# Optimization experiments

Measured on AMD Instinct MI355X. Metric: run time of the kernel, lower is better.

Reference implementation:

```python
import jax, jax.numpy as jnp
import numpy as np
from jax import lax


def _pairwise_dist(a, b):
    # a: (T, D), b: (T, D) -> (T, T) Euclidean distances via GEMM trick
    a2 = jnp.sum(a * a, axis=-1)
    b2 = jnp.sum(b * b, axis=-1)
    sq = a2[:, None] + b2[None, :] - 2.0 * (a @ b.T)
    return jnp.sqrt(jnp.maximum(sq, 1e-12))


def _frechet(seq1, seq2):
    cost = _pairwise_dist(seq1, seq2)  # (T, T)
    ca0 = lax.cummax(cost[0])          # first row boundary: running max

    def row_step(prev, cost_row):
        # prev: ca[i-1, :]; cost_row: cost[i, :]
        c0 = jnp.maximum(prev[0], cost_row[0])  # first-column boundary

        def col_step(left, x):
            c, up, diag = x
            val = jnp.maximum(c, jnp.minimum(jnp.minimum(up, left), diag))
            return val, val

        _, rest = lax.scan(col_step, c0, (cost_row[1:], prev[1:], prev[:-1]))
        cur = jnp.concatenate([c0[None], rest])
        return cur, None

    final_row, _ = lax.scan(row_step, ca0, cost[1:])
    return final_row[-1]


def setup_inputs() -> dict:
    key = jax.random.key(0)
    k1, k2 = jax.random.split(key)
    B, T, D = 32, 1024, 64
    pred = jax.random.normal(k1, (B, T, D), dtype=jnp.float32)
    targ = jax.random.normal(k2, (B, T, D), dtype=jnp.float32)
    return {"pred": pred, "targ": targ}


def reference(pred, targ):
    dists = jax.vmap(_frechet)(pred, targ)  # (B,)
    return jnp.mean(dists)
```

## Files before the change

kernel.cpp:

```cpp
#include <hip/hip_runtime.h>
#include <hip/hip_bf16.h>

#define T_LEN 1024
#define D_DIM 64
#define BATCH 32

#define BM 64
#define BN 128

__global__ __launch_bounds__(256, 3) void cost_kernel(const float* __restrict__ pred,
                                                      const float* __restrict__ targ,
                                                      float* __restrict__ cost) {
    const int b = blockIdx.z;
    const float* P = pred + (size_t)b * T_LEN * D_DIM;
    const float* Tg = targ + (size_t)b * T_LEN * D_DIM;
    float* C = cost + (size_t)b * T_LEN * T_LEN;
    const int row0 = blockIdx.y * BM;
    const int col0 = blockIdx.x * BN;

    __shared__ __align__(16) float ps[BM][D_DIM + 4];
    __shared__ __align__(16) float ts[D_DIM][BN + 4];
    __shared__ float p2[BM], t2[BN];

    const int tid = threadIdx.x;

#pragma unroll
    for (int it = 0; it < 4; ++it) {
        int f = tid + 256 * it;
        int row = f >> 4;
        int kc = f & 15;
        float4 v = *(const float4*)(P + (size_t)(row0 + row) * D_DIM + 4 * kc);
        *(float4*)&ps[row][4 * kc] = v;
    }
#pragma unroll
    for (int it = 0; it < 8; ++it) {
        int f = tid + 256 * it;
        int col = f >> 4;
        int kc = f & 15;
        float4 w = *(const float4*)(Tg + (size_t)(col0 + col) * D_DIM + 4 * kc);
        ts[4 * kc + 0][col] = w.x;
        ts[4 * kc + 1][col] = w.y;
        ts[4 * kc + 2][col] = w.z;
        ts[4 * kc + 3][col] = w.w;
    }
    __syncthreads();

    if (tid < 64) {
        float s = 0.0f;
        const float4* pr = (const float4*)&ps[tid][0];
#pragma unroll
        for (int q = 0; q < 16; ++q) {
            float4 v = pr[q];
            s += v.x * v.x; s += v.y * v.y; s += v.z * v.z; s += v.w * v.w;
        }
        p2[tid] = s;
    } else if (tid < 192) {
        int c = tid - 64;
        float s = 0.0f;
#pragma unroll
        for (int k = 0; k < 64; ++k) { float x = ts[k][c]; s += x * x; }
        t2[c] = s;
    }
    __syncthreads();

    const int tx = tid & 31;
    const int ty = tid >> 5;
    const int r0 = 8 * ty, c0 = 4 * tx;

    float acc[8][4];
#pragma unroll
    for (int i = 0; i < 8; ++i)
#pragma unroll
        for (int j = 0; j < 4; ++j) acc[i][j] = 0.0f;

#pragma unroll
    for (int k4 = 0; k4 < 16; ++k4) {
        float4 b0 = *(const float4*)&ts[4 * k4 + 0][c0];
        float4 b1 = *(const float4*)&ts[4 * k4 + 1][c0];
        float4 b2 = *(const float4*)&ts[4 * k4 + 2][c0];
        float4 b3 = *(const float4*)&ts[4 * k4 + 3][c0];
#pragma unroll
        for (int i = 0; i < 8; ++i) {
            float4 a = *(const float4*)&ps[r0 + i][4 * k4];
            acc[i][0] += a.x * b0.x; acc[i][1] += a.x * b0.y; acc[i][2] += a.x * b0.z; acc[i][3] += a.x * b0.w;
            acc[i][0] += a.y * b1.x; acc[i][1] += a.y * b1.y; acc[i][2] += a.y * b1.z; acc[i][3] += a.y * b1.w;
            acc[i][0] += a.z * b2.x; acc[i][1] += a.z * b2.y; acc[i][2] += a.z * b2.z; acc[i][3] += a.z * b2.w;
            acc[i][0] += a.w * b3.x; acc[i][1] += a.w * b3.y; acc[i][2] += a.w * b3.z; acc[i][3] += a.w * b3.w;
        }
    }

    float4 tt = *(const float4*)&t2[c0];
#pragma unroll
    for (int i = 0; i < 8; ++i) {
        float pa = p2[r0 + i];
        float4 o;
        o.x = sqrtf(fmaxf(pa + tt.x - 2.0f * acc[i][0], 1e-12f));
        o.y = sqrtf(fmaxf(pa + tt.y - 2.0f * acc[i][1], 1e-12f));
        o.z = sqrtf(fmaxf(pa + tt.z - 2.0f * acc[i][2], 1e-12f));
        o.w = sqrtf(fmaxf(pa + tt.w - 2.0f * acc[i][3], 1e-12f));
        *(float4*)(C + (size_t)(row0 + r0 + i) * T_LEN + (col0 + c0)) = o;
    }
}

#define PD 8

#define DP_LOAD4(D0, D1, D2, D3, SRC)                                         \
    asm volatile("global_load_dwordx4 %0, %4, off\n\t"                        \
                 "global_load_dwordx4 %1, %4, off offset:16\n\t"              \
                 "global_load_dwordx4 %2, %4, off offset:32\n\t"              \
                 "global_load_dwordx4 %3, %4, off offset:48"                  \
                 : "=&v"(D0), "=&v"(D1), "=&v"(D2), "=&v"(D3)                 \
                 : "v"(SRC))

__global__ __launch_bounds__(64) void dp_kernel(const float* __restrict__ cost,
                                                float* __restrict__ out) {
    const int b = blockIdx.x;
    const int t = threadIdx.x;
    const float INF = __builtin_inff();
    const float* C = cost + (size_t)b * T_LEN * T_LEN + 16 * t;

    float prev[16];
#pragma unroll
    for (int j = 0; j < 16; ++j) prev[j] = INF;
    float right_out = INF;
    float diag_feed = INF;

    float4 pipe[PD][4];

#pragma unroll
    for (int d = 0; d < PD; ++d) {
        int r = d - t; r = r < 0 ? 0 : (r > T_LEN - 1 ? T_LEN - 1 : r);
        const float* src = C + (size_t)r * T_LEN;
        DP_LOAD4(pipe[d][0], pipe[d][1], pipe[d][2], pipe[d][3], src);
    }

    const int S = T_LEN + 63;
    const int NCH = (S + PD - 1) / PD;
    int s = 0;

#define DP_STEP(U)                                                            \
    {                                                                         \
           \
        asm volatile("s_waitcnt vmcnt(28)" ::: "memory");                     \
        __builtin_amdgcn_sched_barrier(0);                                    \
        const float4 q0 = pipe[U][0], q1 = pipe[U][1];                        \
        const float4 q2 = pipe[U][2], q3 = pipe[U][3];                        \
        const int r = s - t;                                                  \
        float inc = __shfl_up(right_out, 1, 64);                              \
        float left = inc, diag = diag_feed;                                   \
        diag_feed = inc;                                                      \
        if (t == 0) { left = (r == 0) ? -INF : INF; diag = INF; }             \
        if (r >= 0 && r < T_LEN) {                                            \
            float cq[16] = {q0.x, q0.y, q0.z, q0.w, q1.x, q1.y, q1.z, q1.w,   \
                            q2.x, q2.y, q2.z, q2.w, q3.x, q3.y, q3.z, q3.w};  \
            float g[16];                                                      \
            g[0] = fmaxf(cq[0], fminf(prev[0], diag));                        \
            _Pragma("unroll")                                                 \
            for (int j = 1; j < 16; ++j)                                      \
                g[j] = fmaxf(cq[j], fminf(prev[j], prev[j - 1]));             \
            float v = left;                                                   \
            _Pragma("unroll")                                                 \
            for (int j = 0; j < 16; ++j) {                                    \
                v = __builtin_amdgcn_fmed3f(v, cq[j], g[j]);                  \
                prev[j] = v;                                                  \
            }                                                                 \
            right_out = v;                                                    \
        }                                                                     \
        __builtin_amdgcn_sched_barrier(0);                                    \
        {                                                                     \
            int rn = s + PD - t;                                              \
            rn = rn < 0 ? 0 : (rn > T_LEN - 1 ? T_LEN - 1 : rn);              \
            const float* src = C + (size_t)rn * T_LEN;                        \
            DP_LOAD4(pipe[U][0], pipe[U][1], pipe[U][2], pipe[U][3], src);    \
        }                                                                     \
        ++s;                                                                  \
    }

    for (int chunk = 0; chunk < NCH; ++chunk) {
        DP_STEP(0)
        DP_STEP(1)
        DP_STEP(2)
        DP_STEP(3)
        DP_STEP(4)
        DP_STEP(5)
        DP_STEP(6)
        DP_STEP(7)
    }
#undef DP_STEP

    asm volatile("s_waitcnt vmcnt(0)" ::: "memory");
    if (t == 63) atomicAdd(out, prev[15] * (1.0f / (float)BATCH));
}

__global__ __launch_bounds__(64) void dp_fused_kernel(const float* __restrict__ pred,
                                                      const float* __restrict__ targ,
                                                      float* __restrict__ out) {
    const int b = blockIdx.x;
    const int t = threadIdx.x;
    const float INF = __builtin_inff();
    const float* P = pred + (size_t)b * T_LEN * D_DIM;
    const float* T = targ + (size_t)b * T_LEN * D_DIM + (size_t)(16 * t) * D_DIM;

    float prev[16];
#pragma unroll
    for (int j = 0; j < 16; ++j) prev[j] = INF;
    float right_out = INF;
    float diag_feed = INF;

    for (int s = 0; s < T_LEN + 63; s++) {
        int r = s - t;
        float inc = __shfl_up(right_out, 1, 64);
        float left = inc, diag = diag_feed;
        diag_feed = inc;
        if (t == 0) { left = (r == 0) ? -INF : INF; diag = INF; }
        if (r >= 0 && r < T_LEN) {
            float4 pr[16];
            const float4* pp = (const float4*)(P + (size_t)r * D_DIM);
#pragma unroll
            for (int q = 0; q < 16; q++) pr[q] = pp[q];
#pragma unroll
            for (int j = 0; j < 16; j++) {
                const float4* tp = (const float4*)(T + (size_t)j * D_DIM);
                float acc = 0.0f;
#pragma unroll
                for (int q = 0; q < 16; q++) {
                    float4 tv = tp[q];
                    float dx = pr[q].x - tv.x; acc += dx * dx;
                    float dy = pr[q].y - tv.y; acc += dy * dy;
                    float dz = pr[q].z - tv.z; acc += dz * dz;
                    float dw = pr[q].w - tv.w; acc += dw * dw;
                }
                float c = sqrtf(fmaxf(acc, 1e-12f));
                float up = prev[j];
                float v = fmaxf(c, fminf(fminf(up, diag), left));
                diag = up; left = v; prev[j] = v;
            }
            right_out = left;
        }
    }
    if (t == 63) atomicAdd(out, prev[15] * (1.0f / (float)BATCH));
}

extern "C" void kernel_launch(void* const* d_in, const int* in_sizes, int n_in,
                              void* d_out, int out_size, void* d_ws, size_t ws_size,
                              hipStream_t stream) {
    const float* pred = (const float*)d_in[0];
    const float* targ = (const float*)d_in[1];
    float* out = (float*)d_out;

    hipMemsetAsync(out, 0, sizeof(float) * out_size, stream);

    const size_t per_batch = (size_t)T_LEN * T_LEN * sizeof(float);
    int bpg = (int)(ws_size / per_batch);
    if (bpg > BATCH) bpg = BATCH;

    if (bpg >= 1) {
        float* cost = (float*)d_ws;
        for (int g0 = 0; g0 < BATCH; g0 += bpg) {
            int gb = (BATCH - g0) < bpg ? (BATCH - g0) : bpg;
            dim3 grid(T_LEN / BN, T_LEN / BM, gb);
            cost_kernel<<<grid, 256, 0, stream>>>(pred + (size_t)g0 * T_LEN * D_DIM,
                                                  targ + (size_t)g0 * T_LEN * D_DIM,
                                                  cost);
            dp_kernel<<<gb, 64, 0, stream>>>(cost, out);
        }
    } else {
        dp_fused_kernel<<<BATCH, 64, 0, stream>>>(pred, targ, out);
    }
}
```

Before: 360.1 us.

## Enlarge cost GEMM tile to 128x128 and restructure DP pipeline registers

The cost kernel's row tile grows from 64 to 128, so each thread now computes an 8x8 register block instead of 8x4, and occupancy is lowered to 2 blocks. This raises arithmetic intensity and halves the number of target-tile reloads. The DP kernel swaps the pipe array for named float4 registers, moves the shuffle ahead of the waitcnt so its latency overlaps the pending loads, and sets launch bounds (64,1). The larger tile raises register and LDS pressure, which may reduce occupancy in the cost kernel.

```diff
diff --git a/kernel.cpp b/kernel.cpp
--- a/kernel.cpp
+++ b/kernel.cpp
@@ -5,10 +5,10 @@
 #define D_DIM 64
 #define BATCH 32
 
-#define BM 64
+#define BM 128
 #define BN 128
 
-__global__ __launch_bounds__(256, 3) void cost_kernel(const float* __restrict__ pred,
+__global__ __launch_bounds__(256, 2) void cost_kernel(const float* __restrict__ pred,
                                                       const float* __restrict__ targ,
                                                       float* __restrict__ cost) {
     const int b = blockIdx.z;
@@ -25,7 +25,7 @@
     const int tid = threadIdx.x;
 
 #pragma unroll
-    for (int it = 0; it < 4; ++it) {
+    for (int it = 0; it < 8; ++it) {
         int f = tid + 256 * it;
         int row = f >> 4;
         int kc = f & 15;
@@ -45,7 +45,7 @@
     }
     __syncthreads();
 
-    if (tid < 64) {
+    if (tid < 128) {
         float s = 0.0f;
         const float4* pr = (const float4*)&ps[tid][0];
 #pragma unroll
@@ -54,8 +54,8 @@
             s += v.x * v.x; s += v.y * v.y; s += v.z * v.z; s += v.w * v.w;
         }
         p2[tid] = s;
-    } else if (tid < 192) {
-        int c = tid - 64;
+    } else {
+        int c = tid - 128;
         float s = 0.0f;
 #pragma unroll
         for (int k = 0; k < 64; ++k) { float x = ts[k][c]; s += x * x; }
@@ -63,42 +63,72 @@
     }
     __syncthreads();
 
-    const int tx = tid & 31;
-    const int ty = tid >> 5;
-    const int r0 = 8 * ty, c0 = 4 * tx;
-
-    float acc[8][4];
+    const int tx = tid & 15;
+    const int ty = tid >> 4;
+    const int cl = 4 * tx;
+    const int ch = 64 + 4 * tx;
+
+    float acc[8][8];
 #pragma unroll
     for (int i = 0; i < 8; ++i)
 #pragma unroll
-        for (int j = 0; j < 4; ++j) acc[i][j] = 0.0f;
+        for (int j = 0; j < 8; ++j) acc[i][j] = 0.0f;
 
 #pragma unroll
     for (int k4 = 0; k4 < 16; ++k4) {
-        float4 b0 = *(const float4*)&ts[4 * k4 + 0][c0];
-        float4 b1 = *(const float4*)&ts[4 * k4 + 1][c0];
-        float4 b2 = *(const float4*)&ts[4 * k4 + 2][c0];
-        float4 b3 = *(const float4*)&ts[4 * k4 + 3][c0];
-#pragma unroll
-        for (int i = 0; i < 8; ++i) {
-            float4 a = *(const float4*)&ps[r0 + i][4 * k4];
-            acc[i][0] += a.x * b0.x; acc[i][1] += a.x * b0.y; acc[i][2] += a.x * b0.z; acc[i][3] += a.x * b0.w;
-            acc[i][0] += a.y * b1.x; acc[i][1] += a.y * b1.y; acc[i][2] += a.y * b1.z; acc[i][3] += a.y * b1.w;
-            acc[i][0] += a.z * b2.x; acc[i][1] += a.z * b2.y; acc[i][2] += a.z * b2.z; acc[i][3] += a.z * b2.w;
-            acc[i][0] += a.w * b3.x; acc[i][1] += a.w * b3.y; acc[i][2] += a.w * b3.z; acc[i][3] += a.w * b3.w;
-        }
-    }
-
-    float4 tt = *(const float4*)&t2[c0];
-#pragma unroll
-    for (int i = 0; i < 8; ++i) {
-        float pa = p2[r0 + i];
-        float4 o;
-        o.x = sqrtf(fmaxf(pa + tt.x - 2.0f * acc[i][0], 1e-12f));
-        o.y = sqrtf(fmaxf(pa + tt.y - 2.0f * acc[i][1], 1e-12f));
-        o.z = sqrtf(fmaxf(pa + tt.z - 2.0f * acc[i][2], 1e-12f));
-        o.w = sqrtf(fmaxf(pa + tt.w - 2.0f * acc[i][3], 1e-12f));
-        *(float4*)(C + (size_t)(row0 + r0 + i) * T_LEN + (col0 + c0)) = o;
+        float4 bl[4], bh[4];
+#pragma unroll
+        for (int kk = 0; kk < 4; ++kk) {
+            bl[kk] = *(const float4*)&ts[4 * k4 + kk][cl];
+            bh[kk] = *(const float4*)&ts[4 * k4 + kk][ch];
+        }
+#pragma unroll
+        for (int ih = 0; ih < 2; ++ih) {
+#pragma unroll
+            for (int i = 0; i < 4; ++i) {
+                const int rr = (ih ? 64 + 4 * ty : 4 * ty) + i;
+                float4 av = *(const float4*)&ps[rr][4 * k4];
+                const float a4[4] = {av.x, av.y, av.z, av.w};
+                float* A = acc[4 * ih + i];
+#pragma unroll
+                for (int kk = 0; kk < 4; ++kk) {
+                    const float* blp = (const float*)&bl[kk];
+                    const float* bhp = (const float*)&bh[kk];
+                    const float ak = a4[kk];
+#pragma unroll
+                    for (int j = 0; j < 4; ++j) {
+                        A[j]     += ak * blp[j];
+                        A[4 + j] += ak * bhp[j];
+                    }
+                }
+            }
+        }
+    }
+
+    float4 tlo = *(const float4*)&t2[cl];
+    float4 thi = *(const float4*)&t2[ch];
+    const float* tl = (const float*)&tlo;
+    const float* th = (const float*)&thi;
+#pragma unroll
+    for (int ih = 0; ih < 2; ++ih) {
+#pragma unroll
+        for (int i = 0; i < 4; ++i) {
+            const int rr = (ih ? 64 + 4 * ty : 4 * ty) + i;
+            const float pa = p2[rr];
+            float* A = acc[4 * ih + i];
+            float4 o1, o2;
+            o1.x = sqrtf(fmaxf(pa + tl[0] - 2.0f * A[0], 1e-12f));
+            o1.y = sqrtf(fmaxf(pa + tl[1] - 2.0f * A[1], 1e-12f));
+            o1.z = sqrtf(fmaxf(pa + tl[2] - 2.0f * A[2], 1e-12f));
+            o1.w = sqrtf(fmaxf(pa + tl[3] - 2.0f * A[3], 1e-12f));
+            o2.x = sqrtf(fmaxf(pa + th[0] - 2.0f * A[4], 1e-12f));
+            o2.y = sqrtf(fmaxf(pa + th[1] - 2.0f * A[5], 1e-12f));
+            o2.z = sqrtf(fmaxf(pa + th[2] - 2.0f * A[6], 1e-12f));
+            o2.w = sqrtf(fmaxf(pa + th[3] - 2.0f * A[7], 1e-12f));
+            float* Crow = C + (size_t)(row0 + rr) * T_LEN + col0;
+            *(float4*)(Crow + cl) = o1;
+            *(float4*)(Crow + ch) = o2;
+        }
     }
 }
 
@@ -112,8 +142,8 @@
                  : "=&v"(D0), "=&v"(D1), "=&v"(D2), "=&v"(D3)                 \
                  : "v"(SRC))
 
-__global__ __launch_bounds__(64) void dp_kernel(const float* __restrict__ cost,
-                                                float* __restrict__ out) {
+__global__ __launch_bounds__(64, 1) void dp_kernel(const float* __restrict__ cost,
+                                                   float* __restrict__ out) {
     const int b = blockIdx.x;
     const int t = threadIdx.x;
     const float INF = __builtin_inff();
@@ -125,34 +155,41 @@
     float right_out = INF;
     float diag_feed = INF;
 
-    float4 pipe[PD][4];
-
-#pragma unroll
-    for (int d = 0; d < PD; ++d) {
-        int r = d - t; r = r < 0 ? 0 : (r > T_LEN - 1 ? T_LEN - 1 : r);
-        const float* src = C + (size_t)r * T_LEN;
-        DP_LOAD4(pipe[d][0], pipe[d][1], pipe[d][2], pipe[d][3], src);
-    }
+    float4 A0, A1, A2, A3, B0, B1, B2, B3, C0_, C1_, C2_, C3_, D0_, D1_, D2_, D3_;
+    float4 E0, E1, E2, E3, F0, F1, F2, F3, G0, G1, G2, G3, H0, H1, H2, H3;
+
+#define DP_PROLOG(D, P0, P1, P2, P3)                                          \
+    {                                                                         \
+        int r = (D) - t; r = r < 0 ? 0 : r;                                   \
+        const float* src = C + (size_t)r * T_LEN;                             \
+        DP_LOAD4(P0, P1, P2, P3, src);                                        \
+    }
+    DP_PROLOG(0, A0, A1, A2, A3)
+    DP_PROLOG(1, B0, B1, B2, B3)
+    DP_PROLOG(2, C0_, C1_, C2_, C3_)
+    DP_PROLOG(3, D0_, D1_, D2_, D3_)
+    DP_PROLOG(4, E0, E1, E2, E3)
+    DP_PROLOG(5, F0, F1, F2, F3)
+    DP_PROLOG(6, G0, G1, G2, G3)
+    DP_PROLOG(7, H0, H1, H2, H3)
+#undef DP_PROLOG
 
     const int S = T_LEN + 63;
     const int NCH = (S + PD - 1) / PD;
     int s = 0;
 
-#define DP_STEP(U)                                                            \
+#define DP_STEP(P0, P1, P2, P3)                                               \
     {                                                                         \
-           \
+        float inc = __shfl_up(right_out, 1, 64);                              \
         asm volatile("s_waitcnt vmcnt(28)" ::: "memory");                     \
         __builtin_amdgcn_sched_barrier(0);                                    \
-        const float4 q0 = pipe[U][0], q1 = pipe[U][1];                        \
-        const float4 q2 = pipe[U][2], q3 = pipe[U][3];                        \
         const int r = s - t;                                                  \
-        float inc = __shfl_up(right_out, 1, 64);                              \
         float left = inc, diag = diag_feed;                                   \
         diag_feed = inc;                                                      \
         if (t == 0) { left = (r == 0) ? -INF : INF; diag = INF; }             \
         if (r >= 0 && r < T_LEN) {                                            \
-            float cq[16] = {q0.x, q0.y, q0.z, q0.w, q1.x, q1.y, q1.z, q1.w,   \
-                            q2.x, q2.y, q2.z, q2.w, q3.x, q3.y, q3.z, q3.w};  \
+            float cq[16] = {P0.x, P0.y, P0.z, P0.w, P1.x, P1.y, P1.z, P1.w,   \
+                            P2.x, P2.y, P2.z, P2.w, P3.x, P3.y, P3.z, P3.w};  \
             float g[16];                                                      \
             g[0] = fmaxf(cq[0], fminf(prev[0], diag));                        \
             _Pragma("unroll")                                                 \
@@ -171,20 +208,20 @@
             int rn = s + PD - t;                                              \
             rn = rn < 0 ? 0 : (rn > T_LEN - 1 ? T_LEN - 1 : rn);              \
             const float* src = C + (size_t)rn * T_LEN;                        \
-            DP_LOAD4(pipe[U][0], pipe[U][1], pipe[U][2], pipe[U][3], src);    \
+            DP_LOAD4(P0, P1, P2, P3, src);                                    \
         }                                                                     \
         ++s;                                                                  \
     }
 
     for (int chunk = 0; chunk < NCH; ++chunk) {
-        DP_STEP(0)
-        DP_STEP(1)
-        DP_STEP(2)
-        DP_STEP(3)
-        DP_STEP(4)
-        DP_STEP(5)
-        DP_STEP(6)
-        DP_STEP(7)
+        DP_STEP(A0, A1, A2, A3)
+        DP_STEP(B0, B1, B2, B3)
+        DP_STEP(C0_, C1_, C2_, C3_)
+        DP_STEP(D0_, D1_, D2_, D3_)
+        DP_STEP(E0, E1, E2, E3)
+        DP_STEP(F0, F1, F2, F3)
+        DP_STEP(G0, G1, G2, G3)
+        DP_STEP(H0, H1, H2, H3)
     }
 #undef DP_STEP
 
```

New measurement: 367.7 us. 2.1% more time.
